# Optimization experiments

Hardware: AMD Instinct MI355X
Metric: run time of the kernel (lower is better)

The kernel has to match this reference:

```python
import jax, jax.numpy as jnp
import numpy as np

B, S, HID = 1, 2048, 2880
H, KV, D = 64, 8, 64
WINDOW = 128
SCALE = D ** -0.5
NEG_INF = jnp.float32(-1e30)


def _rope_cos_sin():
    # realistic RoPE tables over full head_dim (HF rotate_half convention)
    inv_freq = 1.0 / (10000.0 ** (np.arange(0, D, 2, dtype=np.float32) / D))
    t = np.arange(S, dtype=np.float32)
    freqs = np.outer(t, inv_freq)                      # [S, D/2]
    emb = np.concatenate([freqs, freqs], axis=-1)      # [S, D]
    return jnp.asarray(np.cos(emb))[None], jnp.asarray(np.sin(emb))[None]


def setup_inputs() -> dict:
    key = jax.random.key(0)
    ks = jax.random.split(key, 10)
    cos, sin = _rope_cos_sin()
    sd = lambda fan_in: 1.0 / np.sqrt(fan_in)
    return {
        "hidden_states": jax.random.normal(ks[0], (B, S, HID), jnp.float32),
        "cos": cos, "sin": sin,
        "Wq": jax.random.normal(ks[1], (HID, H * D), jnp.float32) * sd(HID),
        "bq": jax.random.normal(ks[2], (H * D,), jnp.float32) * 0.02,
        "Wk": jax.random.normal(ks[3], (HID, KV * D), jnp.float32) * sd(HID),
        "bk": jax.random.normal(ks[4], (KV * D,), jnp.float32) * 0.02,
        "Wv": jax.random.normal(ks[5], (HID, KV * D), jnp.float32) * sd(HID),
        "bv": jax.random.normal(ks[6], (KV * D,), jnp.float32) * 0.02,
        "Wo": jax.random.normal(ks[7], (H * D, HID), jnp.float32) * sd(H * D),
        "bo": jax.random.normal(ks[8], (HID,), jnp.float32) * 0.02,
        "sinks": jax.random.normal(ks[9], (H,), jnp.float32),
    }


def _rotate_half(x):
    x1, x2 = jnp.split(x, 2, axis=-1)
    return jnp.concatenate([-x2, x1], axis=-1)


def _forward(hidden_states, cos, sin, Wq, bq, Wk, bk, Wv, bv, Wo, bo, sinks):
    q = (hidden_states @ Wq + bq).reshape(B, S, H, D)
    k = (hidden_states @ Wk + bk).reshape(B, S, KV, D)
    v = (hidden_states @ Wv + bv).reshape(B, S, KV, D)
    # RoPE with explicit cos/sin, unsqueeze at head dim (bsnd layout)
    c, s = cos[:, :, None, :], sin[:, :, None, :]
    q = q * c + _rotate_half(q) * s
    k = k * c + _rotate_half(k) * s
    # GQA: expand kv heads to match query heads
    k = jnp.repeat(k, H // KV, axis=2)
    v = jnp.repeat(v, H // KV, axis=2)
    scores = jnp.einsum("bqhd,bkhd->bhqk", q, k) * SCALE  # [B,H,S,S]
    i = jnp.arange(S)[:, None]
    j = jnp.arange(S)[None, :]
    allowed = (j <= i) & (j > i - WINDOW)                  # causal + sliding window
    scores = jnp.where(allowed, scores, NEG_INF)
    # sink-augmented softmax: sinks act as an extra logit per head, dropped after norm
    m = jnp.maximum(scores.max(axis=-1), sinks[None, :, None])  # [B,H,S]
    p = jnp.exp(scores - m[..., None])                      # [B,H,S,S]
    denom = p.sum(axis=-1) + jnp.exp(sinks[None, :, None] - m)  # [B,H,S]
    attn = jnp.einsum("bhqk,bkhd->bqhd", p, v) / denom.transpose(0, 2, 1)[..., None]
    return attn.reshape(B, S, H * D) @ Wo + bo


def reference(hidden_states, cos, sin, Wq, bq, Wk, bk, Wv, bv, Wo, bo, sinks):
    return _forward(hidden_states, cos, sin, Wq, bq, Wk, bk, Wv, bv, Wo, bo, sinks)
```

## Files before the change

kernel.cpp:

```cpp
#include <hip/hip_runtime.h>

typedef unsigned short u16;
typedef __bf16 bf16x8 __attribute__((ext_vector_type(8)));
typedef float f32x4 __attribute__((ext_vector_type(4)));

constexpr int SEQ = 2048;
constexpr int HIDN = 2880;
constexpr int NQKV = 5120;
constexpr float SCALE = 0.125f;
constexpr float NEG_INF = -1e30f;

#define ASM_VMCNT(n)  asm volatile("s_waitcnt vmcnt(" #n ")" ::: "memory")
#define ASM_LGKM(n)   asm volatile("s_waitcnt lgkmcnt(" #n ")" ::: "memory")
#define ASM_BARRIER() asm volatile("s_barrier" ::: "memory")
#define SCHEDBAR()    __builtin_amdgcn_sched_barrier(0)

__device__ __forceinline__ u16 f2bf(float f) {
  unsigned int u = __builtin_bit_cast(unsigned int, f);
  u += 0x7FFFu + ((u >> 16) & 1u);
  return (u16)(u >> 16);
}
__device__ __forceinline__ float bf2f(u16 h) {
  unsigned int u = ((unsigned int)h) << 16;
  return __builtin_bit_cast(float, u);
}
__device__ __forceinline__ void async_load16(const void* g, void* l) {
  __builtin_amdgcn_global_load_lds(
      (const __attribute__((address_space(1))) unsigned int*)g,
      (__attribute__((address_space(3))) unsigned int*)l, 16, 0, 0);
}
__device__ __forceinline__ f32x4 DSR(unsigned addr) {
  f32x4 d;
  asm volatile("ds_read_b128 %0, %1" : "=v"(d) : "v"(addr));
  return d;
}
__device__ __forceinline__ bf16x8 asbf(f32x4 v) { return __builtin_bit_cast(bf16x8, v); }

__global__ __launch_bounds__(256) void conv_f2b(const float* __restrict__ in,
                                                u16* __restrict__ out, long n4) {
  long i = (long)blockIdx.x * 256 + threadIdx.x;
  if (i >= n4) return;
  float4 v = ((const float4*)in)[i];
  u16 o0 = f2bf(v.x), o1 = f2bf(v.y), o2 = f2bf(v.z), o3 = f2bf(v.w);
  out[i * 4 + 0] = o0; out[i * 4 + 1] = o1; out[i * 4 + 2] = o2; out[i * 4 + 3] = o3;
}

__global__ __launch_bounds__(256) void transpose_f2b(const float* __restrict__ in,
                                                     u16* __restrict__ out,
                                                     int R, int C, int ostride) {
  __shared__ float tile[32][33];
  int c0 = blockIdx.x * 32, r0 = blockIdx.y * 32;
  int tx = threadIdx.x & 31, ty = threadIdx.x >> 5;
#pragma unroll
  for (int i = 0; i < 32; i += 8)
    tile[ty + i][tx] = in[(long)(r0 + ty + i) * C + c0 + tx];
  __syncthreads();
#pragma unroll
  for (int i = 0; i < 32; i += 8)
    out[(long)(c0 + ty + i) * ostride + r0 + tx] = f2bf(tile[tx][ty + i]);
}

__global__ __launch_bounds__(256) void concat_bias(const float* bq, const float* bk,
                                                   const float* bv, float* out) {
  int t = blockIdx.x * 256 + threadIdx.x;
  if (t < 4096) out[t] = bq[t];
  else if (t < 4608) out[t] = bk[t - 4096];
  else if (t < 5120) out[t] = bv[t - 4608];
}

template <bool OUT_BF16>
__global__ __launch_bounds__(512, 4) void gemm_w8(const u16* __restrict__ A,
                                                  const u16* __restrict__ B,
                                                  const float* __restrict__ bias,
                                                  void* __restrict__ Cout,
                                                  int N, int K) {
  __shared__ u16 lds[2 * 12288];
  const int tid = threadIdx.x, lane = tid & 63, wid = tid >> 6;
  const int wm = wid >> 2, wn = wid & 3;
  const int lr = lane & 15, lk = lane >> 4;

  const int gm = gridDim.x;
  int nwg = gm * gridDim.y;
  int bid = blockIdx.y * gm + blockIdx.x;
  int q8 = nwg >> 3, r8 = nwg & 7;
  int xcd = bid & 7, seq = bid >> 3;
  int swz = (xcd < r8 ? xcd * (q8 + 1) : r8 * (q8 + 1) + (xcd - r8) * q8) + seq;
  const long brow = (long)(swz % gm) * 128;
  const long bcol = (long)(swz / gm) * 256;
  const int nkt = K >> 5;

  const int c1 = tid + 512;
  const u16* As0 = A + (brow + (tid >> 2)) * (long)K + ((tid & 3) ^ ((tid >> 3) & 3)) * 8;
  const u16* Bs0 = B + (bcol + (tid >> 2)) * (long)K + ((tid & 3) ^ ((tid >> 3) & 3)) * 8;
  const u16* Bs1 = B + (bcol + (c1 >> 2)) * (long)K + ((c1 & 3) ^ ((c1 >> 3) & 3)) * 8;
  char* L = (char*)lds;
  auto stage = [&](int kt, int b) {
    long ko = (long)kt * 32;
    char* d = L + b * 24576;
    async_load16(As0 + ko, d + tid * 16);
    async_load16(Bs0 + ko, d + 8192 + tid * 16);
    async_load16(Bs1 + ko, d + 8192 + c1 * 16);
  };

  const unsigned lds0 = (unsigned)(size_t)L;
  const unsigned xs = (unsigned)((lk ^ ((lr >> 1) & 3)) << 4);
  const unsigned aoff = lds0 + (unsigned)((wm * 64 + lr) * 64) + xs;
  const unsigned boff = lds0 + 8192u + (unsigned)((wn * 64 + lr) * 64) + xs;

  f32x4 acc[4][4] = {};
  stage(0, 0);

  for (int t = 0; t < nkt; ++t) {
    const int b = t & 1;
    if (t + 1 < nkt) { stage(t + 1, b ^ 1); ASM_VMCNT(3); }
    else             { ASM_VMCNT(0); }
    ASM_BARRIER();

    const unsigned ab = aoff + (unsigned)(b * 24576);
    const unsigned bb = boff + (unsigned)(b * 24576);
    f32x4 af[4], bf4[4];
#pragma unroll
    for (int m = 0; m < 4; ++m) af[m] = DSR(ab + m * 1024u);
#pragma unroll
    for (int n = 0; n < 4; ++n) bf4[n] = DSR(bb + n * 1024u);
    ASM_LGKM(0); SCHEDBAR();
    __builtin_amdgcn_s_setprio(1);
#pragma unroll
    for (int m = 0; m < 4; ++m)
#pragma unroll
      for (int n = 0; n < 4; ++n)
        acc[m][n] = __builtin_amdgcn_mfma_f32_16x16x32_bf16(asbf(af[m]), asbf(bf4[n]), acc[m][n], 0, 0, 0);
    __builtin_amdgcn_s_setprio(0);
    ASM_BARRIER();
  }

#pragma unroll
  for (int m = 0; m < 4; ++m) {
    long row = brow + wm * 64 + m * 16 + lk * 4;
#pragma unroll
    for (int n = 0; n < 4; ++n) {
      long col = bcol + wn * 64 + n * 16 + lr;
      if (col < N) {
        float bv = bias[col];
#pragma unroll
        for (int r = 0; r < 4; ++r) {
          float v = acc[m][n][r] + bv;
          if (OUT_BF16) ((u16*)Cout)[(row + r) * (long)N + col] = f2bf(v);
          else          ((float*)Cout)[(row + r) * (long)N + col] = v;
        }
      }
    }
  }
}

__global__ __launch_bounds__(256) void rope_kernel(u16* __restrict__ QKV,
                                                   const float* __restrict__ cosb,
                                                   const float* __restrict__ sinb) {
  long idx = (long)blockIdx.x * 256 + threadIdx.x;
  if (idx >= (long)SEQ * 72 * 32) return;
  int d = idx & 31;
  int h = (int)((idx >> 5) % 72);
  int s = (int)(idx / (72 * 32));
  int col = (h < 64) ? h * 64 : 4096 + (h - 64) * 64;
  u16* p = QKV + (long)s * NQKV + col;
  float x1 = bf2f(p[d]), x2 = bf2f(p[d + 32]);
  float c = cosb[s * 64 + d], sn = sinb[s * 64 + d];
  p[d]      = f2bf(x1 * c - x2 * sn);
  p[d + 32] = f2bf(x2 * c + x1 * sn);
}

__global__ __launch_bounds__(256, 1) void attn_kernel(const u16* __restrict__ QKV,
                                                      const float* __restrict__ sinks,
                                                      u16* __restrict__ Oa) {
  __shared__ u16 Ks[64 * 64];
  __shared__ u16 Vt[64 * 64];
  __shared__ u16 Ps[4][64 * 72];
  const int tid = threadIdx.x, wid = tid >> 6, lane = tid & 63;
  const int lr = lane & 15, lk = lane >> 4;
  const int i0 = blockIdx.x * 64;
  const int h = blockIdx.y * 4 + wid;
  const int g = h >> 3;

  bf16x8 qf[4][2];
#pragma unroll
  for (int m = 0; m < 4; ++m)
#pragma unroll
    for (int kc = 0; kc < 2; ++kc)
      qf[m][kc] = *(const bf16x8*)&QKV[(long)(i0 + m * 16 + lr) * NQKV + h * 64 + kc * 32 + lk * 8];

  const float sinkh = sinks[h];
  float mrun[4][4], lrun[4][4];
  f32x4 oacc[4][4] = {};
#pragma unroll
  for (int m = 0; m < 4; ++m)
#pragma unroll
    for (int r = 0; r < 4; ++r) { mrun[m][r] = sinkh; lrun[m][r] = 0.f; }

  const int jb0 = (i0 >= 128) ? (i0 - 128) : 0;
  for (int jb = jb0; jb <= i0; jb += 64) {
#pragma unroll
    for (int i = 0; i < 2; ++i) {
      int c = wid * 128 + i * 64 + lane;
      int row = c >> 3, sp = c & 7;
      int ssrc = sp ^ (row & 7);
      async_load16(QKV + (long)(jb + row) * NQKV + 4096 + g * 64 + ssrc * 8,
                   ((char*)Ks) + c * 16);
    }
    {
      int j0 = (tid & 31) * 2, d0 = (tid >> 5) * 8;
      const u16* vp = QKV + (long)(jb + j0) * NQKV + 4608 + g * 64 + d0;
      int4 rv0 = *(const int4*)vp;
      int4 rv1 = *(const int4*)(vp + NQKV);
      const u16* a0 = (const u16*)&rv0;
      const u16* a1 = (const u16*)&rv1;
#pragma unroll
      for (int e = 0; e < 8; ++e) {
        int d = d0 + e;
        unsigned val = (unsigned)a0[e] | ((unsigned)a1[e] << 16);
        int byt = d * 128 + ((((j0 >> 3) ^ (d & 7)) << 4)) + ((j0 & 7) * 2);
        *(unsigned*)((char*)Vt + byt) = val;
      }
    }
    __syncthreads();

    f32x4 sf[4][4] = {};
    __builtin_amdgcn_s_setprio(1);
#pragma unroll
    for (int kc = 0; kc < 2; ++kc) {
      bf16x8 kf[4];
#pragma unroll
      for (int cf = 0; cf < 4; ++cf) {
        int row = cf * 16 + lr;
        kf[cf] = *(const bf16x8*)((const char*)Ks + row * 128 + (((kc * 4 + lk) ^ (lr & 7)) << 4));
      }
#pragma unroll
      for (int m = 0; m < 4; ++m)
#pragma unroll
        for (int cf = 0; cf < 4; ++cf)
          sf[m][cf] = __builtin_amdgcn_mfma_f32_16x16x32_bf16(qf[m][kc], kf[cf], sf[m][cf], 0, 0, 0);
    }
    __builtin_amdgcn_s_setprio(0);

#pragma unroll
    for (int m = 0; m < 4; ++m) {
      float rmax[4];
#pragma unroll
      for (int r = 0; r < 4; ++r) {
        int i = i0 + m * 16 + lk * 4 + r;
        float mx = NEG_INF;
#pragma unroll
        for (int cf = 0; cf < 4; ++cf) {
          int j = jb + cf * 16 + lr;
          float v = sf[m][cf][r] * SCALE;
          bool ok = (j <= i) && (j > i - 128);
          v = ok ? v : NEG_INF;
          sf[m][cf][r] = v;
          mx = fmaxf(mx, v);
        }
#pragma unroll
        for (int off = 1; off < 16; off <<= 1) mx = fmaxf(mx, __shfl_xor(mx, off, 64));
        rmax[r] = mx;
      }
#pragma unroll
      for (int r = 0; r < 4; ++r) {
        float mnew = fmaxf(mrun[m][r], rmax[r]);
        float corr = __expf(mrun[m][r] - mnew);
        mrun[m][r] = mnew;
        float rsum = 0.f;
#pragma unroll
        for (int cf = 0; cf < 4; ++cf) {
          float p = __expf(sf[m][cf][r] - mnew);
          sf[m][cf][r] = p;
          rsum += p;
        }
#pragma unroll
        for (int off = 1; off < 16; off <<= 1) rsum += __shfl_xor(rsum, off, 64);
        lrun[m][r] = lrun[m][r] * corr + rsum;
#pragma unroll
        for (int dn = 0; dn < 4; ++dn) oacc[m][dn][r] *= corr;
      }
    }

#pragma unroll
    for (int m = 0; m < 4; ++m)
#pragma unroll
      for (int cf = 0; cf < 4; ++cf)
#pragma unroll
        for (int r = 0; r < 4; ++r)
          Ps[wid][(m * 16 + lk * 4 + r) * 72 + cf * 16 + lr] = f2bf(sf[m][cf][r]);
    __syncthreads();

    __builtin_amdgcn_s_setprio(1);
#pragma unroll
    for (int kc = 0; kc < 2; ++kc) {
      bf16x8 pf[4], vf[4];
#pragma unroll
      for (int m = 0; m < 4; ++m)
        pf[m] = *(const bf16x8*)&Ps[wid][(m * 16 + lr) * 72 + kc * 32 + lk * 8];
#pragma unroll
      for (int dn = 0; dn < 4; ++dn) {
        int row = dn * 16 + lr;
        vf[dn] = *(const bf16x8*)((const char*)Vt + row * 128 + (((kc * 4 + lk) ^ (lr & 7)) << 4));
      }
#pragma unroll
      for (int m = 0; m < 4; ++m)
#pragma unroll
        for (int dn = 0; dn < 4; ++dn)
          oacc[m][dn] = __builtin_amdgcn_mfma_f32_16x16x32_bf16(pf[m], vf[dn], oacc[m][dn], 0, 0, 0);
    }
    __builtin_amdgcn_s_setprio(0);
    __syncthreads();
  }

#pragma unroll
  for (int m = 0; m < 4; ++m)
#pragma unroll
    for (int r = 0; r < 4; ++r) {
      float denom = lrun[m][r] + __expf(sinkh - mrun[m][r]);
      float inv = 1.f / denom;
      long row = i0 + m * 16 + lk * 4 + r;
#pragma unroll
      for (int dn = 0; dn < 4; ++dn)
        Oa[row * 4096 + h * 64 + dn * 16 + lr] = f2bf(oacc[m][dn][r] * inv);
    }
}

extern "C" void kernel_launch(void* const* d_in, const int* in_sizes, int n_in,
                              void* d_out, int out_size, void* d_ws, size_t ws_size,
                              hipStream_t stream) {
  const float* X    = (const float*)d_in[0];
  const float* cosb = (const float*)d_in[1];
  const float* sinb = (const float*)d_in[2];
  const float* Wq   = (const float*)d_in[3];
  const float* bq   = (const float*)d_in[4];
  const float* Wk   = (const float*)d_in[5];
  const float* bk   = (const float*)d_in[6];
  const float* Wv   = (const float*)d_in[7];
  const float* bv   = (const float*)d_in[8];
  const float* Wo   = (const float*)d_in[9];
  const float* bo   = (const float*)d_in[10];
  const float* sinks = (const float*)d_in[11];

  char* ws = (char*)d_ws;
  size_t off = 0;
  auto alloc = [&](size_t bytes) -> void* {
    void* p = ws + off;
    off += (bytes + 255) & ~(size_t)255;
    return p;
  };
  u16*   Xb    = (u16*)alloc((size_t)SEQ * HIDN * 2);
  u16*   Wqkv  = (u16*)alloc((size_t)NQKV * HIDN * 2);
  u16*   Wot   = (u16*)alloc((size_t)3072 * 4096 * 2);
  float* bqkv  = (float*)alloc((size_t)NQKV * 4);
  u16*   QKV   = (u16*)alloc((size_t)SEQ * NQKV * 2);
  u16*   Ab    = (u16*)alloc((size_t)SEQ * 4096 * 2);
  (void)ws_size; (void)in_sizes; (void)n_in; (void)out_size;

  conv_f2b<<<(SEQ * HIDN / 4 + 255) / 256, 256, 0, stream>>>(X, Xb, (long)SEQ * HIDN / 4);
  transpose_f2b<<<dim3(4096 / 32, HIDN / 32), 256, 0, stream>>>(Wq, Wqkv, HIDN, 4096, HIDN);
  transpose_f2b<<<dim3(512 / 32, HIDN / 32), 256, 0, stream>>>(Wk, Wqkv + (size_t)4096 * HIDN, HIDN, 512, HIDN);
  transpose_f2b<<<dim3(512 / 32, HIDN / 32), 256, 0, stream>>>(Wv, Wqkv + (size_t)4608 * HIDN, HIDN, 512, HIDN);
  transpose_f2b<<<dim3(HIDN / 32, 4096 / 32), 256, 0, stream>>>(Wo, Wot, 4096, HIDN, 4096);
  concat_bias<<<(NQKV + 255) / 256, 256, 0, stream>>>(bq, bk, bv, bqkv);
  gemm_w8<true><<<dim3(SEQ / 128, NQKV / 256), 512, 0, stream>>>(Xb, Wqkv, bqkv, QKV, NQKV, HIDN);
  rope_kernel<<<(int)(((long)SEQ * 72 * 32 + 255) / 256), 256, 0, stream>>>(QKV, cosb, sinb);
  attn_kernel<<<dim3(SEQ / 64, 64 / 4), 256, 0, stream>>>(QKV, sinks, Ab);
  gemm_w8<false><<<dim3(SEQ / 128, 3072 / 256), 512, 0, stream>>>(Ab, Wot, bo, (float*)d_out, HIDN, 4096);
}
```

Before: 253.1 us.

## Use 256x256 GEMM tiles with ping-pong quadrant pipeline and split-K output projection

Replaces the 128x256 double-buffered GEMM with a 256x256 tile kernel that splits the LDS into A/B half-tiles and interleaves per-half async loads with quadrant MFMA blocks. This raises arithmetic intensity and overlaps global loads with compute. The output projection uses split-K across two z-slices, with partial results written to d_out and to the reused Wqkv buffer, followed by a combine kernel that adds the bias. The cost is fewer workgroups for the QKV GEMM (160), an extra pass over the fp32 output, and reliance on the even-nkt assumption.

```diff
diff --git a/kernel.cpp b/kernel.cpp
--- a/kernel.cpp
+++ b/kernel.cpp
@@ -68,13 +68,14 @@
   else if (t < 5120) out[t] = bv[t - 4608];
 }
 
-template <bool OUT_BF16>
-__global__ __launch_bounds__(512, 4) void gemm_w8(const u16* __restrict__ A,
-                                                  const u16* __restrict__ B,
-                                                  const float* __restrict__ bias,
-                                                  void* __restrict__ Cout,
-                                                  int N, int K) {
-  __shared__ u16 lds[2 * 12288];
+template <int MODE>
+__global__ __launch_bounds__(512, 2) void gemm8p(const u16* __restrict__ A,
+                                                 const u16* __restrict__ Bp,
+                                                 const float* __restrict__ bias,
+                                                 void* __restrict__ out0,
+                                                 float* __restrict__ out1,
+                                                 int N, int Kst, int nkt) {
+  __shared__ u16 lds[32768];
   const int tid = threadIdx.x, lane = tid & 63, wid = tid >> 6;
   const int wm = wid >> 2, wn = wid & 3;
   const int lr = lane & 15, lk = lane >> 4;
@@ -85,72 +86,131 @@
   int q8 = nwg >> 3, r8 = nwg & 7;
   int xcd = bid & 7, seq = bid >> 3;
   int swz = (xcd < r8 ? xcd * (q8 + 1) : r8 * (q8 + 1) + (xcd - r8) * q8) + seq;
-  const long brow = (long)(swz % gm) * 128;
+  const long brow = (long)(swz % gm) * 256;
   const long bcol = (long)(swz / gm) * 256;
-  const int nkt = K >> 5;
-
-  const int c1 = tid + 512;
-  const u16* As0 = A + (brow + (tid >> 2)) * (long)K + ((tid & 3) ^ ((tid >> 3) & 3)) * 8;
-  const u16* Bs0 = B + (bcol + (tid >> 2)) * (long)K + ((tid & 3) ^ ((tid >> 3) & 3)) * 8;
-  const u16* Bs1 = B + (bcol + (c1 >> 2)) * (long)K + ((c1 & 3) ^ ((c1 >> 3) & 3)) * 8;
+  const long kbase = (MODE == 1) ? (long)blockIdx.z * nkt * 32 : 0;
+
   char* L = (char*)lds;
-  auto stage = [&](int kt, int b) {
-    long ko = (long)kt * 32;
-    char* d = L + b * 24576;
-    async_load16(As0 + ko, d + tid * 16);
-    async_load16(Bs0 + ko, d + 8192 + tid * 16);
-    async_load16(Bs1 + ko, d + 8192 + c1 * 16);
+  const int r0 = tid >> 2;
+  const int srck = ((tid & 3) ^ ((tid >> 3) & 3)) * 8;
+  auto stage1 = [&](int kt, int h) {
+    const u16* s;
+    if (h < 2) s = A  + (brow + h * 128 + r0) * (long)Kst + kbase + (long)kt * 32 + srck;
+    else       s = Bp + (bcol + (h - 2) * 128 + r0) * (long)Kst + kbase + (long)kt * 32 + srck;
+    async_load16(s, L + ((kt & 1) * 4 + h) * 8192 + tid * 16);
   };
 
   const unsigned lds0 = (unsigned)(size_t)L;
-  const unsigned xs = (unsigned)((lk ^ ((lr >> 1) & 3)) << 4);
-  const unsigned aoff = lds0 + (unsigned)((wm * 64 + lr) * 64) + xs;
-  const unsigned boff = lds0 + 8192u + (unsigned)((wn * 64 + lr) * 64) + xs;
-
-  f32x4 acc[4][4] = {};
-  stage(0, 0);
-
-  for (int t = 0; t < nkt; ++t) {
-    const int b = t & 1;
-    if (t + 1 < nkt) { stage(t + 1, b ^ 1); ASM_VMCNT(3); }
-    else             { ASM_VMCNT(0); }
-    ASM_BARRIER();
-
-    const unsigned ab = aoff + (unsigned)(b * 24576);
-    const unsigned bb = boff + (unsigned)(b * 24576);
-    f32x4 af[4], bf4[4];
-#pragma unroll
-    for (int m = 0; m < 4; ++m) af[m] = DSR(ab + m * 1024u);
-#pragma unroll
-    for (int n = 0; n < 4; ++n) bf4[n] = DSR(bb + n * 1024u);
-    ASM_LGKM(0); SCHEDBAR();
-    __builtin_amdgcn_s_setprio(1);
-#pragma unroll
-    for (int m = 0; m < 4; ++m)
-#pragma unroll
-      for (int n = 0; n < 4; ++n)
-        acc[m][n] = __builtin_amdgcn_mfma_f32_16x16x32_bf16(asbf(af[m]), asbf(bf4[n]), acc[m][n], 0, 0, 0);
-    __builtin_amdgcn_s_setprio(0);
+  const unsigned xk = (unsigned)((lk ^ ((lr >> 1) & 3)) << 4);
+  const unsigned raB = lds0 + (unsigned)(wm * 8192 + lr * 64) + xk;
+  const unsigned rbB = lds0 + 16384u + (unsigned)((wn >> 1) * 8192 + ((wn & 1) * 64 + lr) * 64) + xk;
+
+  f32x4 acc[8][4] = {};
+  auto readA4 = [&](int db, int mh, f32x4* d) {
+#pragma unroll
+    for (int mf = 0; mf < 4; ++mf)
+      d[mf] = DSR(raB + (unsigned)(db * 32768 + mh * 4096 + mf * 1024));
+  };
+  auto readB2 = [&](int db, int nh, f32x4* d) {
+#pragma unroll
+    for (int nf = 0; nf < 2; ++nf)
+      d[nf] = DSR(rbB + (unsigned)(db * 32768 + nh * 2048 + nf * 1024));
+  };
+  auto quad8 = [&](int mb, int nb, const f32x4* af, const f32x4* bf) {
+#pragma unroll
+    for (int mf = 0; mf < 4; ++mf)
+#pragma unroll
+      for (int nf = 0; nf < 2; ++nf)
+        acc[mb + mf][nb + nf] = __builtin_amdgcn_mfma_f32_16x16x32_bf16(
+            asbf(af[mf]), asbf(bf[nf]), acc[mb + mf][nb + nf], 0, 0, 0);
+  };
+
+  stage1(0, 0); stage1(0, 1); stage1(0, 2); stage1(0, 3);
+  stage1(1, 2); stage1(1, 3);
+  ASM_VMCNT(2);
+  ASM_BARRIER();
+
+  const int niter = nkt >> 1;
+  for (int it = 0; it < niter; ++it) {
+    const int E = it * 2;
+    const bool sE2 = (E + 2 < nkt), sO2 = (E + 3 < nkt);
+    f32x4 a0[4], a1[4], b0[2], b1[2];
+    readA4(0, 0, a0); readB2(0, 0, b0);
+    stage1(E + 1, 0);
+    ASM_BARRIER(); ASM_LGKM(0); SCHEDBAR();
+    __builtin_amdgcn_s_setprio(1); quad8(0, 0, a0, b0); __builtin_amdgcn_s_setprio(0);
+    ASM_BARRIER();
+    readB2(0, 1, b1);
+    stage1(E + 1, 1);
+    ASM_BARRIER(); ASM_LGKM(0); SCHEDBAR();
+    __builtin_amdgcn_s_setprio(1); quad8(0, 2, a0, b1); __builtin_amdgcn_s_setprio(0);
+    ASM_BARRIER();
+    readA4(0, 1, a1);
+    if (sE2) stage1(E + 2, 2);
+    ASM_BARRIER(); ASM_LGKM(0); SCHEDBAR();
+    __builtin_amdgcn_s_setprio(1); quad8(4, 2, a1, b1); __builtin_amdgcn_s_setprio(0);
+    ASM_BARRIER();
+    if (sE2) { stage1(E + 2, 3); ASM_VMCNT(2); } else { ASM_VMCNT(0); }
+    ASM_BARRIER(); SCHEDBAR();
+    __builtin_amdgcn_s_setprio(1); quad8(4, 0, a1, b0); __builtin_amdgcn_s_setprio(0);
+    ASM_BARRIER();
+    readA4(1, 0, a0); readB2(1, 0, b0);
+    if (sE2) stage1(E + 2, 0);
+    ASM_BARRIER(); ASM_LGKM(0); SCHEDBAR();
+    __builtin_amdgcn_s_setprio(1); quad8(0, 0, a0, b0); __builtin_amdgcn_s_setprio(0);
+    ASM_BARRIER();
+    readB2(1, 1, b1);
+    if (sE2) stage1(E + 2, 1);
+    ASM_BARRIER(); ASM_LGKM(0); SCHEDBAR();
+    __builtin_amdgcn_s_setprio(1); quad8(0, 2, a0, b1); __builtin_amdgcn_s_setprio(0);
+    ASM_BARRIER();
+    readA4(1, 1, a1);
+    if (sO2) stage1(E + 3, 2);
+    ASM_BARRIER(); ASM_LGKM(0); SCHEDBAR();
+    __builtin_amdgcn_s_setprio(1); quad8(4, 2, a1, b1); __builtin_amdgcn_s_setprio(0);
+    ASM_BARRIER();
+    if (sO2) { stage1(E + 3, 3); ASM_VMCNT(2); } else { ASM_VMCNT(0); }
+    ASM_BARRIER(); SCHEDBAR();
+    __builtin_amdgcn_s_setprio(1); quad8(4, 0, a1, b0); __builtin_amdgcn_s_setprio(0);
     ASM_BARRIER();
   }
 
 #pragma unroll
-  for (int m = 0; m < 4; ++m) {
-    long row = brow + wm * 64 + m * 16 + lk * 4;
-#pragma unroll
-    for (int n = 0; n < 4; ++n) {
-      long col = bcol + wn * 64 + n * 16 + lr;
+  for (int mf = 0; mf < 8; ++mf) {
+    long row = brow + wm * 128 + mf * 16 + lk * 4;
+#pragma unroll
+    for (int nf = 0; nf < 4; ++nf) {
+      long col = bcol + wn * 64 + nf * 16 + lr;
       if (col < N) {
-        float bv = bias[col];
-#pragma unroll
-        for (int r = 0; r < 4; ++r) {
-          float v = acc[m][n][r] + bv;
-          if (OUT_BF16) ((u16*)Cout)[(row + r) * (long)N + col] = f2bf(v);
-          else          ((float*)Cout)[(row + r) * (long)N + col] = v;
+        if (MODE == 0) {
+          float bv = bias[col];
+#pragma unroll
+          for (int r = 0; r < 4; ++r)
+            ((u16*)out0)[(row + r) * (long)N + col] = f2bf(acc[mf][nf][r] + bv);
+        } else {
+          float* o = (blockIdx.z == 0) ? (float*)out0 : out1;
+#pragma unroll
+          for (int r = 0; r < 4; ++r)
+            o[(row + r) * (long)N + col] = acc[mf][nf][r];
         }
       }
     }
   }
+}
+
+__global__ __launch_bounds__(256) void combine_out(const float* __restrict__ P1,
+                                                   const float* __restrict__ bias,
+                                                   float* __restrict__ out) {
+  long i = (long)blockIdx.x * 256 + threadIdx.x;
+  if (i >= (long)SEQ * HIDN / 4) return;
+  int c4 = (int)(i % (HIDN / 4));
+  float4 p0 = ((const float4*)out)[i];
+  float4 p1 = ((const float4*)P1)[i];
+  float4 b = ((const float4*)bias)[c4];
+  float4 r;
+  r.x = p0.x + p1.x + b.x; r.y = p0.y + p1.y + b.y;
+  r.z = p0.z + p1.z + b.z; r.w = p0.w + p1.w + b.w;
+  ((float4*)out)[i] = r;
 }
 
 __global__ __launch_bounds__(256) void rope_kernel(u16* __restrict__ QKV,
@@ -354,6 +414,7 @@
   float* bqkv  = (float*)alloc((size_t)NQKV * 4);
   u16*   QKV   = (u16*)alloc((size_t)SEQ * NQKV * 2);
   u16*   Ab    = (u16*)alloc((size_t)SEQ * 4096 * 2);
+  float* Pt1 = (float*)Wqkv;
   (void)ws_size; (void)in_sizes; (void)n_in; (void)out_size;
 
   conv_f2b<<<(SEQ * HIDN / 4 + 255) / 256, 256, 0, stream>>>(X, Xb, (long)SEQ * HIDN / 4);
@@ -362,8 +423,9 @@
   transpose_f2b<<<dim3(512 / 32, HIDN / 32), 256, 0, stream>>>(Wv, Wqkv + (size_t)4608 * HIDN, HIDN, 512, HIDN);
   transpose_f2b<<<dim3(HIDN / 32, 4096 / 32), 256, 0, stream>>>(Wo, Wot, 4096, HIDN, 4096);
   concat_bias<<<(NQKV + 255) / 256, 256, 0, stream>>>(bq, bk, bv, bqkv);
-  gemm_w8<true><<<dim3(SEQ / 128, NQKV / 256), 512, 0, stream>>>(Xb, Wqkv, bqkv, QKV, NQKV, HIDN);
+  gemm8p<0><<<dim3(8, 20, 1), 512, 0, stream>>>(Xb, Wqkv, bqkv, QKV, nullptr, NQKV, HIDN, 90);
   rope_kernel<<<(int)(((long)SEQ * 72 * 32 + 255) / 256), 256, 0, stream>>>(QKV, cosb, sinb);
   attn_kernel<<<dim3(SEQ / 64, 64 / 4), 256, 0, stream>>>(QKV, sinks, Ab);
-  gemm_w8<false><<<dim3(SEQ / 128, 3072 / 256), 512, 0, stream>>>(Ab, Wot, bo, (float*)d_out, HIDN, 4096);
-}
+  gemm8p<1><<<dim3(8, 12, 2), 512, 0, stream>>>(Ab, Wot, nullptr, d_out, Pt1, HIDN, 4096, 64);
+  combine_out<<<(SEQ * HIDN / 4 + 255) / 256, 256, 0, stream>>>(Pt1, bo, (float*)d_out);
+}
```

Result: no change. 251.8 us (-0.5%).
